# Kernel tuning notes

Measured on AMD Instinct MI355X. Metric: run time of the kernel, lower is better.

Reference implementation:

```python
import jax, jax.numpy as jnp
import numpy as np

D = 768

def setup_inputs() -> dict:
    key = jax.random.key(0)
    ks = jax.random.split(key, 8)
    s = 1.0 / np.sqrt(D)
    return {
        "sentence_rep": jax.random.normal(ks[0], (32, 512, D), dtype=jnp.float32),
        "comment_rep": jax.random.normal(ks[1], (32, 2048, D), dtype=jnp.float32),
        "Wq": jax.random.uniform(ks[2], (D, D), jnp.float32, -s, s),
        "bq": jax.random.uniform(ks[3], (D,), jnp.float32, -s, s),
        "Wk": jax.random.uniform(ks[4], (D, D), jnp.float32, -s, s),
        "bk": jax.random.uniform(ks[5], (D,), jnp.float32, -s, s),
        "Wv": jax.random.uniform(ks[6], (D, D), jnp.float32, -s, s),
        "bv": jax.random.uniform(ks[7], (D,), jnp.float32, -s, s),
    }

def reference(sentence_rep, comment_rep, Wq, bq, Wk, bk, Wv, bv):
    # query: [B, Lq, D]; key/value: [B, Lk, D]
    query = jnp.einsum('bqd,ed->bqe', sentence_rep, Wq) + bq
    key_ = jnp.einsum('bkd,ed->bke', comment_rep, Wk) + bk
    value = jnp.einsum('bkd,ed->bke', comment_rep, Wv) + bv
    # sum_q (Q K^T) == (sum_q Q) K^T  -> avoids the [B, Lq, Lk] score matrix
    q_sum = query.sum(axis=1)                       # [B, D]
    scores = jnp.einsum('bd,bkd->bk', q_sum, key_)  # [B, Lk]
    alpha = jax.nn.softmax(scores, axis=-1)         # [B, Lk]
    return jnp.einsum('bk,bkd->bd', alpha, value)   # [B, D]
```

## Files before the change

### kernel.cpp

```cpp
#include <hip/hip_runtime.h>
#include <math.h>

#define B 32
#define LQ 512
#define LK 2048
#define D 768
#define D4 192

__global__ __launch_bounds__(192) void k_sum_sent(const float4* __restrict__ sent,
                                                  float* __restrict__ s_sum) {
    int b = blockIdx.x, qc = blockIdx.y;
    int d4 = threadIdx.x;
    const float4* p = sent + ((size_t)b * LQ + (size_t)qc * 64) * D4 + d4;
    float4 acc = make_float4(0.f, 0.f, 0.f, 0.f);
#pragma unroll 4
    for (int q = 0; q < 64; ++q) {
        float4 v = p[(size_t)q * D4];
        acc.x += v.x; acc.y += v.y; acc.z += v.z; acc.w += v.w;
    }
    float* dst = s_sum + b * D + d4 * 4;
    atomicAdd(dst + 0, acc.x);
    atomicAdd(dst + 1, acc.y);
    atomicAdd(dst + 2, acc.z);
    atomicAdd(dst + 3, acc.w);
}

__global__ __launch_bounds__(256) void k_rowdot(const float4* __restrict__ x4,
                                                const float4* __restrict__ W4,
                                                const float* __restrict__ bias,
                                                float bias_scale,
                                                float* __restrict__ y) {
    int w = blockIdx.x * 4 + (threadIdx.x >> 6);
    int lane = threadIdx.x & 63;
    int b = w / D, e = w % D;
    const float4* xr = x4 + (size_t)b * D4;
    const float4* wr = W4 + (size_t)e * D4;
    float acc = 0.f;
#pragma unroll
    for (int i = 0; i < 3; ++i) {
        int idx = lane + i * 64;
        float4 a = xr[idx], q = wr[idx];
        acc += a.x * q.x + a.y * q.y + a.z * q.z + a.w * q.w;
    }
#pragma unroll
    for (int off = 32; off; off >>= 1) acc += __shfl_down(acc, off, 64);
    if (lane == 0) y[w] = acc + bias_scale * bias[e];
}

__global__ __launch_bounds__(256) void k_qsum_Wk(const float* __restrict__ q_sum,
                                                 const float* __restrict__ Wk,
                                                 float* __restrict__ wk) {
    int b = blockIdx.x;
    int d = blockIdx.y * 256 + threadIdx.x;
    const float* qs = q_sum + b * D;
    float acc = 0.f;
#pragma unroll 8
    for (int e = 0; e < D; ++e)
        acc += qs[e] * Wk[(size_t)e * D + d];
    wk[b * D + d] = acc;
}

__global__ __launch_bounds__(256) void k_scores(const float4* __restrict__ com4,
                                                const float4* __restrict__ wk4,
                                                float* __restrict__ scores) {
    int w = blockIdx.x * 4 + (threadIdx.x >> 6);
    int lane = threadIdx.x & 63;
    int b = w >> 11, k = w & 2047;
    const float4* c = com4 + ((size_t)b * LK + k) * D4;
    const float4* q = wk4 + (size_t)b * D4;
    float acc = 0.f;
#pragma unroll
    for (int i = 0; i < 3; ++i) {
        int idx = lane + i * 64;
        float4 a = c[idx], v = q[idx];
        acc += a.x * v.x + a.y * v.y + a.z * v.z + a.w * v.w;
    }
#pragma unroll
    for (int off = 32; off; off >>= 1) acc += __shfl_down(acc, off, 64);
    if (lane == 0) scores[w] = acc;
}

__global__ __launch_bounds__(256) void k_softmax(const float* __restrict__ scores,
                                                 float* __restrict__ alpha) {
    __shared__ float redm[4];
    __shared__ float reds[4];
    int b = blockIdx.x, tid = threadIdx.x;
    int lane = tid & 63, wid = tid >> 6;
    const float* s = scores + b * LK;
    float v[8];
    float m = -INFINITY;
#pragma unroll
    for (int i = 0; i < 8; ++i) { v[i] = s[tid + i * 256]; m = fmaxf(m, v[i]); }
#pragma unroll
    for (int off = 1; off < 64; off <<= 1) m = fmaxf(m, __shfl_xor(m, off, 64));
    if (lane == 0) redm[wid] = m;
    __syncthreads();
    float mall = fmaxf(fmaxf(redm[0], redm[1]), fmaxf(redm[2], redm[3]));
    float part = 0.f;
    float e[8];
#pragma unroll
    for (int i = 0; i < 8; ++i) { e[i] = expf(v[i] - mall); part += e[i]; }
#pragma unroll
    for (int off = 1; off < 64; off <<= 1) part += __shfl_xor(part, off, 64);
    if (lane == 0) reds[wid] = part;
    __syncthreads();
    float total = reds[0] + reds[1] + reds[2] + reds[3];
    float inv = 1.f / total;
#pragma unroll
    for (int i = 0; i < 8; ++i) alpha[b * LK + tid + i * 256] = e[i] * inv;
}

__global__ __launch_bounds__(192) void k_ctx(const float4* __restrict__ com4,
                                             const float* __restrict__ alpha,
                                             float* __restrict__ ctx) {
    int b = blockIdx.x, kc = blockIdx.y;
    int e4 = threadIdx.x;
    const float4* c = com4 + ((size_t)b * LK + (size_t)kc * 256) * D4 + e4;
    const float* a = alpha + b * LK + kc * 256;
    float4 acc = make_float4(0.f, 0.f, 0.f, 0.f);
#pragma unroll 4
    for (int k = 0; k < 256; ++k) {
        float w = a[k];
        float4 v = c[(size_t)k * D4];
        acc.x += w * v.x; acc.y += w * v.y; acc.z += w * v.z; acc.w += w * v.w;
    }
    float* dst = ctx + b * D + e4 * 4;
    atomicAdd(dst + 0, acc.x);
    atomicAdd(dst + 1, acc.y);
    atomicAdd(dst + 2, acc.z);
    atomicAdd(dst + 3, acc.w);
}

extern "C" void kernel_launch(void* const* d_in, const int* in_sizes, int n_in,
                              void* d_out, int out_size, void* d_ws, size_t ws_size,
                              hipStream_t stream) {
    const float* sent = (const float*)d_in[0];
    const float* com  = (const float*)d_in[1];
    const float* Wq   = (const float*)d_in[2];
    const float* bq   = (const float*)d_in[3];
    const float* Wk   = (const float*)d_in[4];
    const float* Wv   = (const float*)d_in[6];
    const float* bv   = (const float*)d_in[7];
    float* out = (float*)d_out;

    float* ws = (float*)d_ws;
    float* s_sum  = ws;
    float* ctx    = ws + 24576;
    float* q_sum  = ws + 49152;
    float* wk     = ws + 73728;
    float* scores = ws + 98304;
    float* alpha  = ws + 163840;

    hipMemsetAsync(s_sum, 0, 2 * 24576 * sizeof(float), stream);

    k_sum_sent<<<dim3(B, 8), 192, 0, stream>>>((const float4*)sent, s_sum);

    k_rowdot<<<6144, 256, 0, stream>>>((const float4*)s_sum, (const float4*)Wq,
                                       bq, (float)LQ, q_sum);

    k_qsum_Wk<<<dim3(B, 3), 256, 0, stream>>>(q_sum, Wk, wk);

    k_scores<<<16384, 256, 0, stream>>>((const float4*)com, (const float4*)wk, scores);

    k_softmax<<<B, 256, 0, stream>>>(scores, alpha);

    k_ctx<<<dim3(B, 8), 192, 0, stream>>>((const float4*)com, alpha, ctx);

    k_rowdot<<<6144, 256, 0, stream>>>((const float4*)ctx, (const float4*)Wv,
                                       bv, 1.0f, out);
}
```

Baseline: 416.0 us.

## Fuse scores, softmax and context into single-pass online-softmax attention with split merge

Replaces the separate scores, softmax and weighted-sum kernels with one kernel that reads each comment row once, computes its score and keeps an online-softmax running max, sum and weighted accumulator per wave. Per-chunk partial results are merged in a small follow-up kernel. This halves the reads of the large comment tensor and removes the scores/alpha round trips and atomics. It also spreads the sentence-sum kernel over more blocks. In exchange there are branchy per-row rescaling and shared-memory reductions, and only 1024 blocks for the main pass.

Result: faster. 399.3 us (-4.0%).

```diff
diff --git a/kernel.cpp b/kernel.cpp
--- a/kernel.cpp
+++ b/kernel.cpp
@@ -6,15 +6,16 @@
 #define LK 2048
 #define D 768
 #define D4 192
+#define NC 32
 
 __global__ __launch_bounds__(192) void k_sum_sent(const float4* __restrict__ sent,
                                                   float* __restrict__ s_sum) {
     int b = blockIdx.x, qc = blockIdx.y;
     int d4 = threadIdx.x;
-    const float4* p = sent + ((size_t)b * LQ + (size_t)qc * 64) * D4 + d4;
+    const float4* p = sent + ((size_t)b * LQ + (size_t)qc * 16) * D4 + d4;
     float4 acc = make_float4(0.f, 0.f, 0.f, 0.f);
-#pragma unroll 4
-    for (int q = 0; q < 64; ++q) {
+#pragma unroll
+    for (int q = 0; q < 16; ++q) {
         float4 v = p[(size_t)q * D4];
         acc.x += v.x; acc.y += v.y; acc.z += v.z; acc.w += v.w;
     }
@@ -60,75 +61,97 @@
     wk[b * D + d] = acc;
 }
 
-__global__ __launch_bounds__(256) void k_scores(const float4* __restrict__ com4,
-                                                const float4* __restrict__ wk4,
-                                                float* __restrict__ scores) {
-    int w = blockIdx.x * 4 + (threadIdx.x >> 6);
-    int lane = threadIdx.x & 63;
-    int b = w >> 11, k = w & 2047;
-    const float4* c = com4 + ((size_t)b * LK + k) * D4;
-    const float4* q = wk4 + (size_t)b * D4;
-    float acc = 0.f;
+__global__ __launch_bounds__(256) void k_attn(const float4* __restrict__ com4,
+                                              const float* __restrict__ wk,
+                                              float* __restrict__ pv,
+                                              float* __restrict__ pm,
+                                              float* __restrict__ pl) {
+    __shared__ float sm[4], sl[4];
+    __shared__ float sacc[4][D];
+    int b = blockIdx.x, chunk = blockIdx.y;
+    int tid = threadIdx.x, lane = tid & 63, w = tid >> 6;
+
+    const float4* q4 = (const float4*)(wk + (size_t)b * D);
+    float4 q0 = q4[lane], q1 = q4[lane + 64], q2 = q4[lane + 128];
+
+    int row0 = chunk * 64 + w * 16;
+    const float4* base = com4 + ((size_t)b * LK + row0) * D4;
+
+    float m = -INFINITY, l = 0.f;
+    float4 A0 = make_float4(0.f, 0.f, 0.f, 0.f);
+    float4 A1 = make_float4(0.f, 0.f, 0.f, 0.f);
+    float4 A2 = make_float4(0.f, 0.f, 0.f, 0.f);
+
+    for (int r = 0; r < 16; ++r) {
+        float4 c0 = base[(size_t)r * D4 + lane];
+        float4 c1 = base[(size_t)r * D4 + lane + 64];
+        float4 c2 = base[(size_t)r * D4 + lane + 128];
+        float s = c0.x * q0.x + c0.y * q0.y + c0.z * q0.z + c0.w * q0.w
+                + c1.x * q1.x + c1.y * q1.y + c1.z * q1.z + c1.w * q1.w
+                + c2.x * q2.x + c2.y * q2.y + c2.z * q2.z + c2.w * q2.w;
 #pragma unroll
-    for (int i = 0; i < 3; ++i) {
-        int idx = lane + i * 64;
-        float4 a = c[idx], v = q[idx];
-        acc += a.x * v.x + a.y * v.y + a.z * v.z + a.w * v.w;
+        for (int off = 32; off; off >>= 1) s += __shfl_xor(s, off, 64);
+        if (s <= m) {
+            float p = __expf(s - m);
+            l += p;
+            A0.x += p * c0.x; A0.y += p * c0.y; A0.z += p * c0.z; A0.w += p * c0.w;
+            A1.x += p * c1.x; A1.y += p * c1.y; A1.z += p * c1.z; A1.w += p * c1.w;
+            A2.x += p * c2.x; A2.y += p * c2.y; A2.z += p * c2.z; A2.w += p * c2.w;
+        } else {
+            float f = __expf(m - s);
+            l = l * f + 1.f;
+            A0.x = A0.x * f + c0.x; A0.y = A0.y * f + c0.y; A0.z = A0.z * f + c0.z; A0.w = A0.w * f + c0.w;
+            A1.x = A1.x * f + c1.x; A1.y = A1.y * f + c1.y; A1.z = A1.z * f + c1.z; A1.w = A1.w * f + c1.w;
+            A2.x = A2.x * f + c2.x; A2.y = A2.y * f + c2.y; A2.z = A2.z * f + c2.z; A2.w = A2.w * f + c2.w;
+            m = s;
+        }
     }
+
+    if (lane == 0) { sm[w] = m; sl[w] = l; }
+    float4* sa = (float4*)sacc[w];
+    sa[lane] = A0; sa[lane + 64] = A1; sa[lane + 128] = A2;
+    __syncthreads();
+
+    float M = fmaxf(fmaxf(sm[0], sm[1]), fmaxf(sm[2], sm[3]));
+    float e0 = __expf(sm[0] - M), e1 = __expf(sm[1] - M);
+    float e2 = __expf(sm[2] - M), e3 = __expf(sm[3] - M);
+    float L = sl[0] * e0 + sl[1] * e1 + sl[2] * e2 + sl[3] * e3;
+
+    int col = tid * 3;
+    float* dst = pv + ((size_t)b * NC + chunk) * D;
 #pragma unroll
-    for (int off = 32; off; off >>= 1) acc += __shfl_down(acc, off, 64);
-    if (lane == 0) scores[w] = acc;
+    for (int j = 0; j < 3; ++j) {
+        int c = col + j;
+        dst[c] = sacc[0][c] * e0 + sacc[1][c] * e1 + sacc[2][c] * e2 + sacc[3][c] * e3;
+    }
+    if (tid == 0) { pm[b * NC + chunk] = M; pl[b * NC + chunk] = L; }
 }
 
-__global__ __launch_bounds__(256) void k_softmax(const float* __restrict__ scores,
-                                                 float* __restrict__ alpha) {
-    __shared__ float redm[4];
-    __shared__ float reds[4];
+__global__ __launch_bounds__(256) void k_merge(const float* __restrict__ pv,
+                                               const float* __restrict__ pm,
+                                               const float* __restrict__ pl,
+                                               float* __restrict__ ctx) {
+    __shared__ float spm[NC], spl[NC];
     int b = blockIdx.x, tid = threadIdx.x;
-    int lane = tid & 63, wid = tid >> 6;
-    const float* s = scores + b * LK;
-    float v[8];
-    float m = -INFINITY;
+    if (tid < NC) { spm[tid] = pm[b * NC + tid]; spl[tid] = pl[b * NC + tid]; }
+    __syncthreads();
+    float M = -INFINITY;
 #pragma unroll
-    for (int i = 0; i < 8; ++i) { v[i] = s[tid + i * 256]; m = fmaxf(m, v[i]); }
+    for (int c = 0; c < NC; ++c) M = fmaxf(M, spm[c]);
+    float L = 0.f;
 #pragma unroll
-    for (int off = 1; off < 64; off <<= 1) m = fmaxf(m, __shfl_xor(m, off, 64));
-    if (lane == 0) redm[wid] = m;
-    __syncthreads();
-    float mall = fmaxf(fmaxf(redm[0], redm[1]), fmaxf(redm[2], redm[3]));
-    float part = 0.f;
-    float e[8];
-#pragma unroll
-    for (int i = 0; i < 8; ++i) { e[i] = expf(v[i] - mall); part += e[i]; }
-#pragma unroll
-    for (int off = 1; off < 64; off <<= 1) part += __shfl_xor(part, off, 64);
-    if (lane == 0) reds[wid] = part;
-    __syncthreads();
-    float total = reds[0] + reds[1] + reds[2] + reds[3];
-    float inv = 1.f / total;
-#pragma unroll
-    for (int i = 0; i < 8; ++i) alpha[b * LK + tid + i * 256] = e[i] * inv;
-}
-
-__global__ __launch_bounds__(192) void k_ctx(const float4* __restrict__ com4,
-                                             const float* __restrict__ alpha,
-                                             float* __restrict__ ctx) {
-    int b = blockIdx.x, kc = blockIdx.y;
-    int e4 = threadIdx.x;
-    const float4* c = com4 + ((size_t)b * LK + (size_t)kc * 256) * D4 + e4;
-    const float* a = alpha + b * LK + kc * 256;
-    float4 acc = make_float4(0.f, 0.f, 0.f, 0.f);
-#pragma unroll 4
-    for (int k = 0; k < 256; ++k) {
-        float w = a[k];
-        float4 v = c[(size_t)k * D4];
-        acc.x += w * v.x; acc.y += w * v.y; acc.z += w * v.z; acc.w += w * v.w;
+    for (int c = 0; c < NC; ++c) L += spl[c] * __expf(spm[c] - M);
+    float inv = 1.f / L;
+    int col = tid * 3;
+    float o0 = 0.f, o1 = 0.f, o2 = 0.f;
+    for (int c = 0; c < NC; ++c) {
+        float e = __expf(spm[c] - M);
+        const float* p = pv + ((size_t)b * NC + c) * D + col;
+        o0 += e * p[0]; o1 += e * p[1]; o2 += e * p[2];
     }
-    float* dst = ctx + b * D + e4 * 4;
-    atomicAdd(dst + 0, acc.x);
-    atomicAdd(dst + 1, acc.y);
-    atomicAdd(dst + 2, acc.z);
-    atomicAdd(dst + 3, acc.w);
+    ctx[b * D + col] = o0 * inv;
+    ctx[b * D + col + 1] = o1 * inv;
+    ctx[b * D + col + 2] = o2 * inv;
 }
 
 extern "C" void kernel_launch(void* const* d_in, const int* in_sizes, int n_in,
@@ -144,27 +167,26 @@
     float* out = (float*)d_out;
 
     float* ws = (float*)d_ws;
-    float* s_sum  = ws;
-    float* ctx    = ws + 24576;
-    float* q_sum  = ws + 49152;
-    float* wk     = ws + 73728;
-    float* scores = ws + 98304;
-    float* alpha  = ws + 163840;
+    float* s_sum = ws;
+    float* q_sum = ws + 24576;
+    float* wk    = ws + 49152;
+    float* ctx   = ws + 73728;
+    float* pm    = ws + 98304;
+    float* pl    = ws + 99328;
+    float* pv    = ws + 100352;
 
-    hipMemsetAsync(s_sum, 0, 2 * 24576 * sizeof(float), stream);
+    hipMemsetAsync(s_sum, 0, 24576 * sizeof(float), stream);
 
-    k_sum_sent<<<dim3(B, 8), 192, 0, stream>>>((const float4*)sent, s_sum);
+    k_sum_sent<<<dim3(B, 32), 192, 0, stream>>>((const float4*)sent, s_sum);
 
     k_rowdot<<<6144, 256, 0, stream>>>((const float4*)s_sum, (const float4*)Wq,
                                        bq, (float)LQ, q_sum);
 
     k_qsum_Wk<<<dim3(B, 3), 256, 0, stream>>>(q_sum, Wk, wk);
 
-    k_scores<<<16384, 256, 0, stream>>>((const float4*)com, (const float4*)wk, scores);
+    k_attn<<<dim3(B, NC), 256, 0, stream>>>((const float4*)com, wk, pv, pm, pl);
 
-    k_softmax<<<B, 256, 0, stream>>>(scores, alpha);
-
-    k_ctx<<<dim3(B, 8), 192, 0, stream>>>((const float4*)com, alpha, ctx);
+    k_merge<<<B, 256, 0, stream>>>(pv, pm, pl, ctx);
 
     k_rowdot<<<6144, 256, 0, stream>>>((const float4*)ctx, (const float4*)Wv,
                                        bv, 1.0f, out);
```
